# Performance work log

Measured on AMD Instinct MI355X. Metric: run time of the kernel, lower is better.

The kernel has to match this reference:

```python
import jax, jax.numpy as jnp
import numpy as np

INPUT_DIM = 362
HIDDEN = 256
STYLE_NUM = 60
OUTFIT_NUM = 49710
BATCH = 16384


def setup_inputs() -> dict:
    key = jax.random.key(0)
    ks = jax.random.split(key, 12)
    f32 = jnp.float32
    return {
        "i_feature": jax.random.normal(ks[0], (BATCH, INPUT_DIM), f32),
        "j_feature": jax.random.normal(ks[1], (BATCH, INPUT_DIM), f32),
        "k_feature": jax.random.normal(ks[2], (BATCH, INPUT_DIM), f32),
        # top_emb / bottom_emb Linear params (stored transposed: x @ W + b)
        "W_top": jax.random.normal(ks[3], (INPUT_DIM, HIDDEN), f32) * 0.05,
        "b_top": jnp.zeros((HIDDEN,), f32),
        "W_bot": jax.random.normal(ks[4], (INPUT_DIM, HIDDEN), f32) * 0.05,
        "b_bot": jnp.zeros((HIDDEN,), f32),
        # NMF factors (forward relu_'s them in place; we relu on use)
        "P_nmf": jax.random.normal(ks[5], (2 * INPUT_DIM, STYLE_NUM), f32),
        "N_nmf": jax.random.normal(ks[6], (2 * INPUT_DIM, STYLE_NUM), f32),
        "H1_nmf": jax.random.normal(ks[7], (STYLE_NUM, OUTFIT_NUM), f32),
        "H2_nmf": jax.random.normal(ks[8], (STYLE_NUM, OUTFIT_NUM), f32),
        "matirx_pos": jax.random.uniform(ks[9], (2 * INPUT_DIM, OUTFIT_NUM), f32),
        "matirx_neg": jax.random.uniform(ks[10], (2 * INPUT_DIM, OUTFIT_NUM), f32),
    }


def _emb(x, W, b):
    # nn.Sequential(Linear, Sigmoid)
    return jax.nn.sigmoid(x @ W + b)


def _style_score(i_f, j_f, styles, W_top, b_top, W_bot, b_bot):
    # Vectorized version of the per-sample loop:
    # squared-distance argmin codebook lookup + gather + rowwise dot.
    outfit = jnp.concatenate([i_f, j_f], axis=1)  # [B, 2D]
    # mean over feature dim of (x - s)^2; constant 1/(2D) scale does not change argmin
    d2 = (jnp.sum(outfit * outfit, axis=1, keepdims=True)
          - 2.0 * (outfit @ styles)
          + jnp.sum(styles * styles, axis=0, keepdims=True))  # [B, S]
    idx = jnp.argmin(d2, axis=1)                               # [B]
    sel = styles.T[idx]                                        # [B, 2D] gather
    top, bot = sel[:, :INPUT_DIM], sel[:, INPUT_DIM:]
    # diag(matmul) == rowwise dot
    return jnp.sum(_emb(top, W_top, b_top) * _emb(bot, W_bot, b_bot), axis=1)  # [B]


def reference(i_feature, j_feature, k_feature, W_top, b_top, W_bot, b_bot,
              P_nmf, N_nmf, H1_nmf, H2_nmf, matirx_pos, matirx_neg):
    Ti = _emb(i_feature, W_top, b_top)   # [B, H]
    Bj = _emb(j_feature, W_bot, b_bot)   # [B, H]
    Bk = _emb(k_feature, W_bot, b_bot)   # [B, H]
    # torch.diag(matmul(Ti, Bj.T)) == rowwise dot (avoids [B,B] intermediate)
    ij_score = jnp.sum(Ti * Bj, axis=1)  # [B]
    ik_score = jnp.sum(Ti * Bk, axis=1)  # [B]

    # forward does relu_ on .data before use
    P = jnp.maximum(P_nmf, 0.0)
    N = jnp.maximum(N_nmf, 0.0)
    H1 = jnp.maximum(H1_nmf, 0.0)
    H2 = jnp.maximum(H2_nmf, 0.0)

    style_ij = _style_score(i_feature, j_feature, P, W_top, b_top, W_bot, b_bot)
    style_ik = _style_score(i_feature, k_feature, N, W_top, b_top, W_bot, b_bot)

    # -mean(log(sigmoid(d))) computed stably
    loss1 = -jnp.mean(jax.nn.log_sigmoid(ij_score - ik_score))
    loss2 = -jnp.mean(jax.nn.log_sigmoid(style_ij - style_ik))
    loss3 = jnp.mean(jnp.square(matirx_pos - P @ H1)
                     + jnp.square(matirx_neg - N @ H2))
    loss = loss1 + loss2 + 0.1 * loss3

    ij_ik = jnp.stack([ij_score, ik_score], axis=1)  # [B, 2]
    auc = jnp.mean((jnp.argmax(ij_ik, axis=1) == 0).astype(jnp.float32))
    return (loss, loss1, loss2, loss3, auc)
```

## Files before the change

kernel.cpp:

```cpp
#include <hip/hip_runtime.h>
#include <math.h>

#define BATCH 16384
#define IND   362
#define KP    384
#define HID   256
#define STY   60
#define NOUT  49710
#define OUTP  49792
#define D2    724
#define D2P   768
#define NSTRIP 777
#define L3_BLOCKS (2 * NSTRIP)

#define NB_SS   120
#define NB_CH   390
#define NB_CW   768
#define NB_CPN  384
#define NB_CF   9216
#define NB_PREP (NB_SS + NB_CH + NB_CW + NB_CPN + NB_CF)

#define NB_EMB  512
#define NB_SA   512
#define NB_MAIN (L3_BLOCKS + NB_EMB + NB_SA)

typedef __bf16 bf16x8 __attribute__((ext_vector_type(8)));
typedef float  floatx4 __attribute__((ext_vector_type(4)));
typedef float  floatx2 __attribute__((ext_vector_type(2)));

__device__ inline floatx4 mfma16(bf16x8 a, bf16x8 b, floatx4 c) {
  return __builtin_amdgcn_mfma_f32_16x16x32_bf16(a, b, c, 0, 0, 0);
}

__device__ inline unsigned short f32_to_bf16(float x) {
  unsigned int u = __float_as_uint(x);
  unsigned int r = (u + 0x7FFFu + ((u >> 16) & 1u)) >> 16;
  return (unsigned short)r;
}

__device__ inline float sigm_fast(float x) { return 1.0f / (1.0f + __expf(-x)); }
__device__ inline float softplusf(float z) { return fmaxf(z, 0.0f) + log1pf(expf(-fabsf(z))); }

__global__ __launch_bounds__(256) void k_prep(
    const float* __restrict__ fi, const float* __restrict__ fj, const float* __restrict__ fk,
    const float* __restrict__ Wt, const float* __restrict__ btop,
    const float* __restrict__ Wb, const float* __restrict__ bbot,
    const float* __restrict__ Pn, const float* __restrict__ Nn,
    const float* __restrict__ H1, const float* __restrict__ H2,
    unsigned short* __restrict__ fbf, unsigned short* __restrict__ wbfT,
    unsigned short* __restrict__ pnbf, unsigned short* __restrict__ pnbfT,
    unsigned short* __restrict__ hbfT,
    float* __restrict__ ss, float* __restrict__ cn) {
  __shared__ float sel[D2];
  __shared__ float shr[4];
  int b = blockIdx.x;
  int t = threadIdx.x;

  if (b < NB_SS) {
    int s  = b % STY;
    int mt = b / STY;
    const float* M = mt ? Nn : Pn;
    float cnp = 0.0f;
    for (int d = t; d < D2; d += 256) {
      float v = fmaxf(M[(size_t)d * STY + s], 0.0f);
      sel[d] = v;
      cnp += v * v;
    }
    __syncthreads();
    float at = btop[t], ab = bbot[t];
    for (int d = 0; d < IND; d++) at = fmaf(sel[d],       Wt[(size_t)d * HID + t], at);
    for (int d = 0; d < IND; d++) ab = fmaf(sel[IND + d], Wb[(size_t)d * HID + t], ab);
    float prod = (1.0f / (1.0f + expf(-at))) * (1.0f / (1.0f + expf(-ab)));
    for (int off = 32; off > 0; off >>= 1) prod += __shfl_xor(prod, off);
    if ((t & 63) == 0) shr[t >> 6] = prod;
    __syncthreads();
    if (t == 0) ss[mt * 64 + s] = shr[0] + shr[1] + shr[2] + shr[3];
    __syncthreads();
    for (int off = 32; off > 0; off >>= 1) cnp += __shfl_xor(cnp, off);
    if ((t & 63) == 0) shr[t >> 6] = cnp;
    __syncthreads();
    if (t == 0) cn[mt * 64 + s] = shr[0] + shr[1] + shr[2] + shr[3];
    return;
  }
  b -= NB_SS;

  if (b < NB_CH) {
    int o = (b % 195) * 256 + t;
    int m = b / 195;
    if (o >= OUTP) return;
    const float* H = m ? H2 : H1;
    unsigned short* dst = hbfT + ((size_t)m * OUTP + o) * 64;
    bool ov = (o < NOUT);
    #pragma unroll
    for (int g = 0; g < 8; g++) {
      unsigned int wv[4];
      #pragma unroll
      for (int e = 0; e < 4; e++) {
        int kk = g * 8 + e * 2;
        float lo = (ov && kk < STY)     ? fmaxf(H[(size_t)kk * NOUT + o], 0.0f) : 0.0f;
        float hi = (ov && kk + 1 < STY) ? fmaxf(H[(size_t)(kk + 1) * NOUT + o], 0.0f) : 0.0f;
        wv[e] = (unsigned)f32_to_bf16(lo) | ((unsigned)f32_to_bf16(hi) << 16);
      }
      uint4 v; v.x = wv[0]; v.y = wv[1]; v.z = wv[2]; v.w = wv[3];
      *(uint4*)(dst + g * 8) = v;
    }
    return;
  }
  b -= NB_CH;

  if (b < NB_CW) {
    int idx = b * 256 + t;
    int k = idx % KP;
    int rem = idx / KP;
    int h = rem % HID;
    int mm = rem / HID;
    const float* W = mm ? Wb : Wt;
    wbfT[idx] = f32_to_bf16(k < IND ? W[(size_t)k * HID + h] : 0.0f);
    return;
  }
  b -= NB_CW;

  if (b < NB_CPN) {
    int u = b * 256 + t;
    int s = u & 63;
    int v = u >> 6;
    int m = (v >= D2P) ? 1 : 0;
    int d = v - m * D2P;
    const float* M = m ? Nn : Pn;
    float x = (d < D2 && s < STY) ? fmaxf(M[(size_t)d * STY + s], 0.0f) : 0.0f;
    unsigned short bb = f32_to_bf16(x);
    pnbf[((size_t)m * D2P + d) * 64 + s] = bb;
    int k = (d < IND) ? d : (d < D2 ? d + 22 : (d < 746 ? d - IND : d));
    pnbfT[((size_t)m * 64 + s) * D2P + k] = bb;
    return;
  }
  b -= NB_CPN;

  {
    long u = (long)b * 256 + t;
    int g = (int)(u % 48);
    long rf = u / 48;
    int row = (int)(rf % BATCH);
    int f = (int)(rf / BATCH);
    const float* src = (f == 0) ? fi : (f == 1 ? fj : fk);
    int d0 = g * 8;
    const float* sp = src + (size_t)row * IND + d0;
    unsigned int wv[4];
    #pragma unroll
    for (int e = 0; e < 4; e++) {
      int dd = d0 + 2 * e;
      float lo = (dd < IND)     ? sp[2 * e]     : 0.0f;
      float hi = (dd + 1 < IND) ? sp[2 * e + 1] : 0.0f;
      wv[e] = (unsigned)f32_to_bf16(lo) | ((unsigned)f32_to_bf16(hi) << 16);
    }
    uint4 v; v.x = wv[0]; v.y = wv[1]; v.z = wv[2]; v.w = wv[3];
    *(uint4*)(fbf + ((size_t)f * BATCH + row) * KP + d0) = v;
  }
}

__global__ __launch_bounds__(256) void k_main(
    const unsigned short* __restrict__ fbf, const unsigned short* __restrict__ wbfT,
    const unsigned short* __restrict__ pnbf, const unsigned short* __restrict__ pnbfT,
    const unsigned short* __restrict__ hbfT,
    const float* __restrict__ btop, const float* __restrict__ bbot,
    const float* __restrict__ cn, const float* __restrict__ ss,
    const float* __restrict__ mp, const float* __restrict__ mn,
    float* __restrict__ sIJ, float* __restrict__ sIK,
    float* __restrict__ stIJ, float* __restrict__ stIK,
    float* __restrict__ partial) {
  __shared__ float shp[4];
  int w = threadIdx.x >> 6, lane = threadIdx.x & 63;
  int m = lane & 15, q = lane >> 4;
  int b = blockIdx.x;

  if (b < L3_BLOCKS) {
    int strip = b % NSTRIP;
    int mat   = b / NSTRIP;
    int o0 = strip * 64;
    const float* M = mat ? mn : mp;
    const unsigned short* Hb = hbfT + (size_t)mat * OUTP * 64;
    const unsigned short* Pb = pnbf + (size_t)mat * D2P * 64;

    bf16x8 a[4][2];
    #pragma unroll
    for (int t = 0; t < 4; t++)
      #pragma unroll
      for (int kc = 0; kc < 2; kc++)
        a[t][kc] = *(const bf16x8*)(Hb + (size_t)(o0 + t * 16 + m) * 64 + kc * 32 + q * 8);

    bool full = (o0 + 64 <= NOUT);
    float local = 0.0f;
    floatx2 pcur[8], pnxt[8];
    #pragma unroll
    for (int i = 0; i < 8; i++) { pcur[i] = (floatx2){0.f, 0.f}; pnxt[i] = (floatx2){0.f, 0.f}; }

    auto LOAD = [&](int dt, floatx2* dst) {
      int d = dt * 16 + m;
      if (d < D2) {
        const float* Mrow = M + (size_t)d * NOUT + o0;
        if (full) {
          #pragma unroll
          for (int t = 0; t < 4; t++) {
            int ob = t * 16 + q * 4;
            dst[2 * t]     = *(const floatx2*)(Mrow + ob);
            dst[2 * t + 1] = *(const floatx2*)(Mrow + ob + 2);
          }
        } else {
          #pragma unroll
          for (int t = 0; t < 4; t++) {
            int ob = t * 16 + q * 4;
            floatx2 v0 = {0.f, 0.f}, v1 = {0.f, 0.f};
            if (o0 + ob     < NOUT) v0[0] = Mrow[ob];
            if (o0 + ob + 1 < NOUT) v0[1] = Mrow[ob + 1];
            if (o0 + ob + 2 < NOUT) v1[0] = Mrow[ob + 2];
            if (o0 + ob + 3 < NOUT) v1[1] = Mrow[ob + 3];
            dst[2 * t] = v0; dst[2 * t + 1] = v1;
          }
        }
      }
    };

    LOAD(w, pcur);
    for (int dt = w; dt < 46; dt += 4) {
      if (dt + 4 < 46) LOAD(dt + 4, pnxt);
      int d0 = dt * 16;
      const unsigned short* bp = Pb + (size_t)(d0 + m) * 64 + q * 8;
      bf16x8 b0 = *(const bf16x8*)(bp);
      bf16x8 b1 = *(const bf16x8*)(bp + 32);
      floatx4 acc[4];
      #pragma unroll
      for (int t = 0; t < 4; t++) {
        acc[t] = (floatx4){0.f, 0.f, 0.f, 0.f};
        acc[t] = mfma16(a[t][0], b0, acc[t]);
        acc[t] = mfma16(a[t][1], b1, acc[t]);
      }
      if (d0 + m < D2) {
        #pragma unroll
        for (int t = 0; t < 4; t++) {
          float e0 = pcur[2 * t][0]     - acc[t][0];
          float e1 = pcur[2 * t][1]     - acc[t][1];
          float e2 = pcur[2 * t + 1][0] - acc[t][2];
          float e3 = pcur[2 * t + 1][1] - acc[t][3];
          local += e0 * e0 + e1 * e1 + e2 * e2 + e3 * e3;
        }
      }
      #pragma unroll
      for (int i = 0; i < 8; i++) pcur[i] = pnxt[i];
    }
    for (int off = 32; off > 0; off >>= 1) local += __shfl_xor(local, off);
    if (lane == 0) shp[w] = local;
    __syncthreads();
    if (threadIdx.x == 0) partial[b] = shp[0] + shp[1] + shp[2] + shp[3];
    return;
  }
  b -= L3_BLOCKS;

  if (b < NB_EMB) {
    int r0 = (b & 255) * 64 + w * 16;
    int hb = (b >> 8) * 128;
    const unsigned short* fi = fbf + (size_t)(r0 + m) * KP + q * 8;
    const unsigned short* fj = fi + (size_t)BATCH * KP;
    const unsigned short* fk = fj + (size_t)BATCH * KP;
    floatx4 accI[8], accJ[8], accK[8];
    #pragma unroll
    for (int nt = 0; nt < 8; nt++) {
      accI[nt] = (floatx4){0.f, 0.f, 0.f, 0.f};
      accJ[nt] = (floatx4){0.f, 0.f, 0.f, 0.f};
      accK[nt] = (floatx4){0.f, 0.f, 0.f, 0.f};
    }
    for (int kc = 0; kc < 12; kc++) {
      bf16x8 ai = *(const bf16x8*)(fi + kc * 32);
      bf16x8 aj = *(const bf16x8*)(fj + kc * 32);
      bf16x8 ak = *(const bf16x8*)(fk + kc * 32);
      #pragma unroll
      for (int nt = 0; nt < 8; nt++) {
        int n = hb + nt * 16 + m;
        const unsigned short* wp = wbfT + (size_t)n * KP + kc * 32 + q * 8;
        bf16x8 bt8 = *(const bf16x8*)(wp);
        bf16x8 bb8 = *(const bf16x8*)(wp + (size_t)HID * KP);
        accI[nt] = mfma16(ai, bt8, accI[nt]);
        accJ[nt] = mfma16(aj, bb8, accJ[nt]);
        accK[nt] = mfma16(ak, bb8, accK[nt]);
      }
    }
    float sij[4] = {0.f, 0.f, 0.f, 0.f}, sik[4] = {0.f, 0.f, 0.f, 0.f};
    #pragma unroll
    for (int nt = 0; nt < 8; nt++) {
      int n = hb + nt * 16 + m;
      float vbt = btop[n], vbb = bbot[n];
      #pragma unroll
      for (int reg = 0; reg < 4; reg++) {
        float ti = sigm_fast(accI[nt][reg] + vbt);
        float tj = sigm_fast(accJ[nt][reg] + vbb);
        float tk = sigm_fast(accK[nt][reg] + vbb);
        sij[reg] += ti * tj;
        sik[reg] += ti * tk;
      }
    }
    #pragma unroll
    for (int reg = 0; reg < 4; reg++) {
      for (int off = 1; off < 16; off <<= 1) {
        sij[reg] += __shfl_xor(sij[reg], off);
        sik[reg] += __shfl_xor(sik[reg], off);
      }
    }
    if (m == 0) {
      #pragma unroll
      for (int reg = 0; reg < 4; reg++) {
        int row = r0 + q * 4 + reg;
        atomicAdd(&sIJ[row], sij[reg]);
        atomicAdd(&sIK[row], sik[reg]);
      }
    }
    return;
  }
  b -= NB_EMB;

  {
    int mat = w & 1;
    int r0 = b * 32 + (w >> 1) * 16;
    const unsigned short* fA = fbf + (size_t)(r0 + m) * KP + q * 8;
    const unsigned short* fB = fA + (size_t)(1 + mat) * BATCH * KP;
    const unsigned short* Bp = pnbfT + (size_t)mat * 64 * D2P + q * 8;
    floatx4 acc[4];
    #pragma unroll
    for (int nt = 0; nt < 4; nt++) acc[nt] = (floatx4){0.f, 0.f, 0.f, 0.f};
    for (int kc = 0; kc < 24; kc++) {
      bf16x8 a = (kc < 12) ? *(const bf16x8*)(fA + kc * 32)
                           : *(const bf16x8*)(fB + (kc - 12) * 32);
      #pragma unroll
      for (int nt = 0; nt < 4; nt++) {
        bf16x8 bb = *(const bf16x8*)(Bp + (size_t)(nt * 16 + m) * D2P + kc * 32);
        acc[nt] = mfma16(a, bb, acc[nt]);
      }
    }
    const float* cnm = cn + mat * 64;
    float bv[4]; int bi[4];
    #pragma unroll
    for (int reg = 0; reg < 4; reg++) { bv[reg] = __builtin_inff(); bi[reg] = 1 << 30; }
    #pragma unroll
    for (int nt = 0; nt < 4; nt++) {
      int s = nt * 16 + m;
      float c = cnm[s & 63];
      #pragma unroll
      for (int reg = 0; reg < 4; reg++) {
        float d2 = (s < STY) ? (c - 2.0f * acc[nt][reg]) : __builtin_inff();
        if (d2 < bv[reg] || (d2 == bv[reg] && s < bi[reg])) { bv[reg] = d2; bi[reg] = s; }
      }
    }
    for (int off = 1; off < 16; off <<= 1) {
      #pragma unroll
      for (int reg = 0; reg < 4; reg++) {
        float ov = __shfl_xor(bv[reg], off);
        int   oi = __shfl_xor(bi[reg], off);
        if (ov < bv[reg] || (ov == bv[reg] && oi < bi[reg])) { bv[reg] = ov; bi[reg] = oi; }
      }
    }
    if (m == 0) {
      float* dst = mat ? stIK : stIJ;
      const float* ssm = ss + mat * 64;
      #pragma unroll
      for (int reg = 0; reg < 4; reg++) dst[r0 + q * 4 + reg] = ssm[bi[reg]];
    }
  }
}

__global__ __launch_bounds__(256) void k_final(
    const float* __restrict__ sIJ, const float* __restrict__ sIK,
    const float* __restrict__ stIJ, const float* __restrict__ stIK,
    const float* __restrict__ l3partial, float* __restrict__ out) {
  int t = threadIdx.x;
  float l1 = 0.f, l2 = 0.f, ac = 0.f;
  for (int r = t; r < BATCH; r += 256) {
    float dij = sIJ[r] - sIK[r];
    l1 += softplusf(-dij);
    if (dij >= 0.0f) ac += 1.0f;
    float dst = stIJ[r] - stIK[r];
    l2 += softplusf(-dst);
  }
  double l3 = 0.0;
  for (int p = t; p < L3_BLOCKS; p += 256) l3 += (double)l3partial[p];
  __shared__ float sh1[4], sh2[4], sh3[4];
  __shared__ double sh4[4];
  for (int off = 32; off > 0; off >>= 1) {
    l1 += __shfl_xor(l1, off);
    l2 += __shfl_xor(l2, off);
    ac += __shfl_xor(ac, off);
    l3 += __shfl_xor(l3, off);
  }
  if ((t & 63) == 0) { sh1[t >> 6] = l1; sh2[t >> 6] = l2; sh3[t >> 6] = ac; sh4[t >> 6] = l3; }
  __syncthreads();
  if (t == 0) {
    double L1 = 0, L2 = 0, AC = 0, L3 = 0;
    for (int i = 0; i < 4; i++) { L1 += sh1[i]; L2 += sh2[i]; AC += sh3[i]; L3 += sh4[i]; }
    L1 /= BATCH; L2 /= BATCH; AC /= BATCH;
    L3 /= ((double)D2 * (double)NOUT);
    out[0] = (float)(L1 + L2 + 0.1 * L3);
    out[1] = (float)L1;
    out[2] = (float)L2;
    out[3] = (float)L3;
    out[4] = (float)AC;
  }
}

extern "C" void kernel_launch(void* const* d_in, const int* in_sizes, int n_in,
                              void* d_out, int out_size, void* d_ws, size_t ws_size,
                              hipStream_t stream) {
  (void)in_sizes; (void)n_in; (void)out_size; (void)ws_size;
  const float* i_f  = (const float*)d_in[0];
  const float* j_f  = (const float*)d_in[1];
  const float* k_f  = (const float*)d_in[2];
  const float* W_t  = (const float*)d_in[3];
  const float* b_t  = (const float*)d_in[4];
  const float* W_b  = (const float*)d_in[5];
  const float* b_b  = (const float*)d_in[6];
  const float* P_n  = (const float*)d_in[7];
  const float* N_n  = (const float*)d_in[8];
  const float* H1   = (const float*)d_in[9];
  const float* H2   = (const float*)d_in[10];
  const float* Mp   = (const float*)d_in[11];
  const float* Mn   = (const float*)d_in[12];
  float* out = (float*)d_out;
  char* ws = (char*)d_ws;

  const size_t OFF_FBF   = 0;
  const size_t OFF_WBFT  = OFF_FBF  + (size_t)3 * BATCH * KP * 2;
  const size_t OFF_PNBF  = OFF_WBFT + (size_t)2 * HID * KP * 2;
  const size_t OFF_PNBFT = OFF_PNBF + (size_t)2 * D2P * 64 * 2;
  const size_t OFF_HBFT  = OFF_PNBFT+ (size_t)2 * 64 * D2P * 2;
  const size_t OFF_SIJ   = OFF_HBFT + (size_t)2 * OUTP * 64 * 2;
  const size_t OFF_SIK   = OFF_SIJ  + (size_t)BATCH * 4;
  const size_t OFF_STIJ  = OFF_SIK  + (size_t)BATCH * 4;
  const size_t OFF_STIK  = OFF_STIJ + (size_t)BATCH * 4;
  const size_t OFF_SS    = OFF_STIK + (size_t)BATCH * 4;
  const size_t OFF_CN    = OFF_SS   + 512;
  const size_t OFF_L3P   = OFF_CN   + 512;

  unsigned short* fbf   = (unsigned short*)(ws + OFF_FBF);
  unsigned short* wbfT  = (unsigned short*)(ws + OFF_WBFT);
  unsigned short* pnbf  = (unsigned short*)(ws + OFF_PNBF);
  unsigned short* pnbfT = (unsigned short*)(ws + OFF_PNBFT);
  unsigned short* hbfT  = (unsigned short*)(ws + OFF_HBFT);
  float*  sIJ  = (float*)(ws + OFF_SIJ);
  float*  sIK  = (float*)(ws + OFF_SIK);
  float*  stIJ = (float*)(ws + OFF_STIJ);
  float*  stIK = (float*)(ws + OFF_STIK);
  float*  ss   = (float*)(ws + OFF_SS);
  float*  cn   = (float*)(ws + OFF_CN);
  float*  l3p  = (float*)(ws + OFF_L3P);

  hipMemsetAsync(ws + OFF_SIJ, 0, (size_t)BATCH * 4 * 2, stream);

  k_prep<<<NB_PREP, 256, 0, stream>>>(i_f, j_f, k_f, W_t, b_t, W_b, b_b,
                                      P_n, N_n, H1, H2,
                                      fbf, wbfT, pnbf, pnbfT, hbfT, ss, cn);
  k_main<<<NB_MAIN, 256, 0, stream>>>(fbf, wbfT, pnbf, pnbfT, hbfT,
                                      b_t, b_b, cn, ss, Mp, Mn,
                                      sIJ, sIK, stIJ, stIK, l3p);
  k_final<<<1, 256, 0, stream>>>(sIJ, sIK, stIJ, stIK, l3p, out);
}
```

Before: 641.0 us.

## Expand NMF reconstruction loss algebraically via Gram matrices instead of forming P@H

The loss3 term is rewritten as sum(M^2) - 2*sum(P ⊙ (M·H^T)) + <P^T P, H H^T>. This avoids reconstructing P@H at every element. The main blocks now stream M once, computing M·H^T with MFMA over output chunks. Extra head blocks compute the 64x64 Gram matrices H·H^T and P^T·P, which are combined in the final kernel. H is also stored row-major in bf16, the embedding blocks are split to a smaller hidden tile, and occupancy hints are added. The risks are cancellation error from subtracting large terms and global atomics from the few long-running head blocks.

```diff
diff --git a/kernel.cpp b/kernel.cpp
--- a/kernel.cpp
+++ b/kernel.cpp
@@ -7,22 +7,27 @@
 #define HID   256
 #define STY   60
 #define NOUT  49710
-#define OUTP  49792
+#define OUTP  49920
 #define D2    724
 #define D2P   768
-#define NSTRIP 777
-#define L3_BLOCKS (2 * NSTRIP)
 
 #define NB_SS   120
-#define NB_CH   390
+#define NB_HR   3120
 #define NB_CW   768
 #define NB_CPN  384
 #define NB_CF   9216
-#define NB_PREP (NB_SS + NB_CH + NB_CW + NB_CPN + NB_CF)
-
-#define NB_EMB  512
+#define NB_PREP (NB_SS + NB_HR + NB_CW + NB_CPN + NB_CF)
+
+#define NB_HH   16
+#define NB_PPB  2
+#define NB_HEAD (NB_HH + NB_PPB)
+#define N_DT    46
+#define N_OC    24
+#define OCHUNK  2080
+#define NB_M    (2 * N_DT * N_OC)
+#define NB_EMB  1024
 #define NB_SA   512
-#define NB_MAIN (L3_BLOCKS + NB_EMB + NB_SA)
+#define NB_MAIN (NB_HEAD + NB_M + NB_EMB + NB_SA)
 
 typedef __bf16 bf16x8 __attribute__((ext_vector_type(8)));
 typedef float  floatx4 __attribute__((ext_vector_type(4)));
@@ -48,8 +53,7 @@
     const float* __restrict__ Pn, const float* __restrict__ Nn,
     const float* __restrict__ H1, const float* __restrict__ H2,
     unsigned short* __restrict__ fbf, unsigned short* __restrict__ wbfT,
-    unsigned short* __restrict__ pnbf, unsigned short* __restrict__ pnbfT,
-    unsigned short* __restrict__ hbfT,
+    unsigned short* __restrict__ pnbfT, unsigned short* __restrict__ hrows,
     float* __restrict__ ss, float* __restrict__ cn) {
   __shared__ float sel[D2];
   __shared__ float shr[4];
@@ -84,29 +88,36 @@
   }
   b -= NB_SS;
 
-  if (b < NB_CH) {
-    int o = (b % 195) * 256 + t;
-    int m = b / 195;
-    if (o >= OUTP) return;
-    const float* H = m ? H2 : H1;
-    unsigned short* dst = hbfT + ((size_t)m * OUTP + o) * 64;
-    bool ov = (o < NOUT);
-    #pragma unroll
-    for (int g = 0; g < 8; g++) {
-      unsigned int wv[4];
-      #pragma unroll
-      for (int e = 0; e < 4; e++) {
-        int kk = g * 8 + e * 2;
-        float lo = (ov && kk < STY)     ? fmaxf(H[(size_t)kk * NOUT + o], 0.0f) : 0.0f;
-        float hi = (ov && kk + 1 < STY) ? fmaxf(H[(size_t)(kk + 1) * NOUT + o], 0.0f) : 0.0f;
-        wv[e] = (unsigned)f32_to_bf16(lo) | ((unsigned)f32_to_bf16(hi) << 16);
-      }
-      uint4 v; v.x = wv[0]; v.y = wv[1]; v.z = wv[2]; v.w = wv[3];
-      *(uint4*)(dst + g * 8) = v;
-    }
-    return;
-  }
-  b -= NB_CH;
+  if (b < NB_HR) {
+    int e = (b * 256 + t) * 8;
+    int row = e / OUTP;
+    int o = e - row * OUTP;
+    int s = row & 63;
+    int mm = row >> 6;
+    const float* H = mm ? H2 : H1;
+    unsigned short* dst = hrows + (size_t)row * OUTP + o;
+    unsigned int wv[4];
+    if (s < STY && o + 8 <= NOUT) {
+      const float* src = H + (size_t)s * NOUT + o;
+      #pragma unroll
+      for (int ee = 0; ee < 4; ee++) {
+        floatx2 v = *(const floatx2*)(src + 2 * ee);
+        wv[ee] = (unsigned)f32_to_bf16(fmaxf(v[0], 0.0f)) |
+                 ((unsigned)f32_to_bf16(fmaxf(v[1], 0.0f)) << 16);
+      }
+    } else {
+      #pragma unroll
+      for (int ee = 0; ee < 4; ee++) {
+        float lo = (s < STY && o + 2 * ee     < NOUT) ? fmaxf(H[(size_t)s * NOUT + o + 2 * ee],     0.0f) : 0.0f;
+        float hi = (s < STY && o + 2 * ee + 1 < NOUT) ? fmaxf(H[(size_t)s * NOUT + o + 2 * ee + 1], 0.0f) : 0.0f;
+        wv[ee] = (unsigned)f32_to_bf16(lo) | ((unsigned)f32_to_bf16(hi) << 16);
+      }
+    }
+    uint4 v; v.x = wv[0]; v.y = wv[1]; v.z = wv[2]; v.w = wv[3];
+    *(uint4*)dst = v;
+    return;
+  }
+  b -= NB_HR;
 
   if (b < NB_CW) {
     int idx = b * 256 + t;
@@ -129,7 +140,6 @@
     const float* M = m ? Nn : Pn;
     float x = (d < D2 && s < STY) ? fmaxf(M[(size_t)d * STY + s], 0.0f) : 0.0f;
     unsigned short bb = f32_to_bf16(x);
-    pnbf[((size_t)m * D2P + d) * 64 + s] = bb;
     int k = (d < IND) ? d : (d < D2 ? d + 22 : (d < 746 ? d - IND : d));
     pnbfT[((size_t)m * 64 + s) * D2P + k] = bb;
     return;
@@ -158,112 +168,176 @@
   }
 }
 
-__global__ __launch_bounds__(256) void k_main(
+__global__ __launch_bounds__(256, 4) void k_main(
     const unsigned short* __restrict__ fbf, const unsigned short* __restrict__ wbfT,
-    const unsigned short* __restrict__ pnbf, const unsigned short* __restrict__ pnbfT,
-    const unsigned short* __restrict__ hbfT,
+    const unsigned short* __restrict__ pnbfT, const unsigned short* __restrict__ hrows,
     const float* __restrict__ btop, const float* __restrict__ bbot,
     const float* __restrict__ cn, const float* __restrict__ ss,
-    const float* __restrict__ mp, const float* __restrict__ mn,
+    const float* __restrict__ mp, const float* __restrict__ mneg,
+    const float* __restrict__ Pn, const float* __restrict__ Nn,
     float* __restrict__ sIJ, float* __restrict__ sIK,
     float* __restrict__ stIJ, float* __restrict__ stIK,
+    float* __restrict__ HHb, float* __restrict__ PPb,
     float* __restrict__ partial) {
   __shared__ float shp[4];
+  __shared__ float red[4096];
   int w = threadIdx.x >> 6, lane = threadIdx.x & 63;
   int m = lane & 15, q = lane >> 4;
   int b = blockIdx.x;
 
-  if (b < L3_BLOCKS) {
-    int strip = b % NSTRIP;
-    int mat   = b / NSTRIP;
-    int o0 = strip * 64;
-    const float* M = mat ? mn : mp;
-    const unsigned short* Hb = hbfT + (size_t)mat * OUTP * 64;
-    const unsigned short* Pb = pnbf + (size_t)mat * D2P * 64;
-
-    bf16x8 a[4][2];
-    #pragma unroll
-    for (int t = 0; t < 4; t++)
-      #pragma unroll
-      for (int kc = 0; kc < 2; kc++)
-        a[t][kc] = *(const bf16x8*)(Hb + (size_t)(o0 + t * 16 + m) * 64 + kc * 32 + q * 8);
-
-    bool full = (o0 + 64 <= NOUT);
-    float local = 0.0f;
-    floatx2 pcur[8], pnxt[8];
-    #pragma unroll
-    for (int i = 0; i < 8; i++) { pcur[i] = (floatx2){0.f, 0.f}; pnxt[i] = (floatx2){0.f, 0.f}; }
-
-    auto LOAD = [&](int dt, floatx2* dst) {
-      int d = dt * 16 + m;
-      if (d < D2) {
-        const float* Mrow = M + (size_t)d * NOUT + o0;
+  if (b < NB_HEAD) {
+    bool isPP = (b >= NB_HH);
+    int mat, chunk, nsteps, stride;
+    const unsigned short* Rb;
+    if (!isPP) { mat = b >> 3; chunk = b & 7; Rb = hrows + (size_t)mat * 64 * OUTP; stride = OUTP; nsteps = 195; }
+    else       { mat = b - NB_HH; chunk = 0; Rb = pnbfT + (size_t)mat * 64 * D2P;  stride = D2P;  nsteps = 24;  }
+    const unsigned short* Rm = Rb + (size_t)m * stride;
+
+    floatx4 acc[4][4];
+    #pragma unroll
+    for (int a2 = 0; a2 < 4; a2++)
+      #pragma unroll
+      for (int b2 = 0; b2 < 4; b2++) acc[a2][b2] = (floatx4){0.f, 0.f, 0.f, 0.f};
+
+    bf16x8 hc[4], hn[4];
+    auto LD = [&](int j, bf16x8* h) {
+      int k = (chunk * nsteps + j) * 32 + q * 8;
+      #pragma unroll
+      for (int st = 0; st < 4; st++)
+        h[st] = *(const bf16x8*)(Rm + (size_t)(st * 16) * stride + k);
+    };
+    int j = w;
+    LD(j, hc);
+    for (; j < nsteps; j += 4) {
+      if (j + 4 < nsteps) LD(j + 4, hn);
+      #pragma unroll
+      for (int a2 = 0; a2 < 4; a2++)
+        #pragma unroll
+        for (int b2 = 0; b2 < 4; b2++)
+          acc[a2][b2] = mfma16(hc[a2], hc[b2], acc[a2][b2]);
+      #pragma unroll
+      for (int st = 0; st < 4; st++) hc[st] = hn[st];
+    }
+    for (int idx = threadIdx.x; idx < 4096; idx += 256) red[idx] = 0.f;
+    __syncthreads();
+    #pragma unroll
+    for (int a2 = 0; a2 < 4; a2++)
+      #pragma unroll
+      for (int b2 = 0; b2 < 4; b2++)
+        #pragma unroll
+        for (int r = 0; r < 4; r++)
+          atomicAdd(&red[(a2 * 16 + q * 4 + r) * 64 + b2 * 16 + m], acc[a2][b2][r]);
+    __syncthreads();
+    float* dst = (isPP ? PPb : HHb) + (size_t)mat * 4096;
+    for (int idx = threadIdx.x; idx < 4096; idx += 256) atomicAdd(&dst[idx], red[idx]);
+    return;
+  }
+  b -= NB_HEAD;
+
+  if (b < NB_M) {
+    int dt  = b % N_DT;
+    int r   = b / N_DT;
+    int oc  = r % N_OC;
+    int mat = r / N_OC;
+    int d0 = dt * 16, o0 = oc * OCHUNK;
+    bool full = (o0 + OCHUNK <= NOUT);
+    int d = d0 + m;
+    bool rowok = (d < D2);
+    const float* Mrow = (mat ? mneg : mp) + (size_t)d * NOUT;
+    const unsigned short* Hbase = hrows + ((size_t)mat * 64 + m) * OUTP;
+
+    floatx4 acc[4];
+    #pragma unroll
+    for (int st = 0; st < 4; st++) acc[st] = (floatx4){0.f, 0.f, 0.f, 0.f};
+    float msq = 0.0f;
+
+    floatx2 mc[4], mnx[4];
+    bf16x8  hc[4], hn[4];
+
+    auto LOADM = [&](int j, floatx2* dst) {
+      int o = o0 + j * 32 + q * 8;
+      if (rowok) {
+        const float* Mr = Mrow + o;
         if (full) {
-          #pragma unroll
-          for (int t = 0; t < 4; t++) {
-            int ob = t * 16 + q * 4;
-            dst[2 * t]     = *(const floatx2*)(Mrow + ob);
-            dst[2 * t + 1] = *(const floatx2*)(Mrow + ob + 2);
-          }
+          dst[0] = *(const floatx2*)(Mr);
+          dst[1] = *(const floatx2*)(Mr + 2);
+          dst[2] = *(const floatx2*)(Mr + 4);
+          dst[3] = *(const floatx2*)(Mr + 6);
         } else {
           #pragma unroll
-          for (int t = 0; t < 4; t++) {
-            int ob = t * 16 + q * 4;
-            floatx2 v0 = {0.f, 0.f}, v1 = {0.f, 0.f};
-            if (o0 + ob     < NOUT) v0[0] = Mrow[ob];
-            if (o0 + ob + 1 < NOUT) v0[1] = Mrow[ob + 1];
-            if (o0 + ob + 2 < NOUT) v1[0] = Mrow[ob + 2];
-            if (o0 + ob + 3 < NOUT) v1[1] = Mrow[ob + 3];
-            dst[2 * t] = v0; dst[2 * t + 1] = v1;
+          for (int e = 0; e < 4; e++) {
+            floatx2 v = {0.f, 0.f};
+            if (o + 2 * e     < NOUT) v[0] = Mr[2 * e];
+            if (o + 2 * e + 1 < NOUT) v[1] = Mr[2 * e + 1];
+            dst[e] = v;
           }
         }
+      } else {
+        #pragma unroll
+        for (int e = 0; e < 4; e++) dst[e] = (floatx2){0.f, 0.f};
       }
     };
-
-    LOAD(w, pcur);
-    for (int dt = w; dt < 46; dt += 4) {
-      if (dt + 4 < 46) LOAD(dt + 4, pnxt);
-      int d0 = dt * 16;
-      const unsigned short* bp = Pb + (size_t)(d0 + m) * 64 + q * 8;
-      bf16x8 b0 = *(const bf16x8*)(bp);
-      bf16x8 b1 = *(const bf16x8*)(bp + 32);
-      floatx4 acc[4];
-      #pragma unroll
-      for (int t = 0; t < 4; t++) {
-        acc[t] = (floatx4){0.f, 0.f, 0.f, 0.f};
-        acc[t] = mfma16(a[t][0], b0, acc[t]);
-        acc[t] = mfma16(a[t][1], b1, acc[t]);
-      }
-      if (d0 + m < D2) {
+    auto LOADH = [&](int j, bf16x8* h) {
+      int o = o0 + j * 32 + q * 8;
+      #pragma unroll
+      for (int st = 0; st < 4; st++)
+        h[st] = *(const bf16x8*)(Hbase + (size_t)(st * 16) * OUTP + o);
+    };
+
+    LOADM(w, mc);
+    LOADH(w, hc);
+    for (int j = w; j < 65; j += 4) {
+      if (j + 4 < 65) { LOADM(j + 4, mnx); LOADH(j + 4, hn); }
+      union { unsigned int u32[4]; bf16x8 v; } cv;
+      #pragma unroll
+      for (int e = 0; e < 4; e++) {
+        msq = fmaf(mc[e][0], mc[e][0], msq);
+        msq = fmaf(mc[e][1], mc[e][1], msq);
+        cv.u32[e] = (unsigned)f32_to_bf16(mc[e][0]) | ((unsigned)f32_to_bf16(mc[e][1]) << 16);
+      }
+      bf16x8 af = cv.v;
+      #pragma unroll
+      for (int st = 0; st < 4; st++) acc[st] = mfma16(af, hc[st], acc[st]);
+      #pragma unroll
+      for (int e = 0; e < 4; e++) mc[e] = mnx[e];
+      #pragma unroll
+      for (int st = 0; st < 4; st++) hc[st] = hn[st];
+    }
+
+    const float* PM = mat ? Nn : Pn;
+    float t2 = 0.0f;
+    #pragma unroll
+    for (int st = 0; st < 4; st++) {
+      int s = st * 16 + m;
+      if (s < STY) {
         #pragma unroll
-        for (int t = 0; t < 4; t++) {
-          float e0 = pcur[2 * t][0]     - acc[t][0];
-          float e1 = pcur[2 * t][1]     - acc[t][1];
-          float e2 = pcur[2 * t + 1][0] - acc[t][2];
-          float e3 = pcur[2 * t + 1][1] - acc[t][3];
-          local += e0 * e0 + e1 * e1 + e2 * e2 + e3 * e3;
+        for (int rg = 0; rg < 4; rg++) {
+          int dd = d0 + q * 4 + rg;
+          if (dd < D2) {
+            float pv = fmaxf(PM[(size_t)dd * STY + s], 0.0f);
+            t2 = fmaf(pv, acc[st][rg], t2);
+          }
         }
       }
-      #pragma unroll
-      for (int i = 0; i < 8; i++) pcur[i] = pnxt[i];
-    }
+    }
+    float local = msq - 2.0f * t2;
     for (int off = 32; off > 0; off >>= 1) local += __shfl_xor(local, off);
     if (lane == 0) shp[w] = local;
     __syncthreads();
     if (threadIdx.x == 0) partial[b] = shp[0] + shp[1] + shp[2] + shp[3];
     return;
   }
-  b -= L3_BLOCKS;
+  b -= NB_M;
 
   if (b < NB_EMB) {
     int r0 = (b & 255) * 64 + w * 16;
-    int hb = (b >> 8) * 128;
+    int hb = (b >> 8) * 64;
     const unsigned short* fi = fbf + (size_t)(r0 + m) * KP + q * 8;
     const unsigned short* fj = fi + (size_t)BATCH * KP;
     const unsigned short* fk = fj + (size_t)BATCH * KP;
-    floatx4 accI[8], accJ[8], accK[8];
-    #pragma unroll
-    for (int nt = 0; nt < 8; nt++) {
+    floatx4 accI[4], accJ[4], accK[4];
+    #pragma unroll
+    for (int nt = 0; nt < 4; nt++) {
       accI[nt] = (floatx4){0.f, 0.f, 0.f, 0.f};
       accJ[nt] = (floatx4){0.f, 0.f, 0.f, 0.f};
       accK[nt] = (floatx4){0.f, 0.f, 0.f, 0.f};
@@ -273,7 +347,7 @@
       bf16x8 aj = *(const bf16x8*)(fj + kc * 32);
       bf16x8 ak = *(const bf16x8*)(fk + kc * 32);
       #pragma unroll
-      for (int nt = 0; nt < 8; nt++) {
+      for (int nt = 0; nt < 4; nt++) {
         int n = hb + nt * 16 + m;
         const unsigned short* wp = wbfT + (size_t)n * KP + kc * 32 + q * 8;
         bf16x8 bt8 = *(const bf16x8*)(wp);
@@ -285,7 +359,7 @@
     }
     float sij[4] = {0.f, 0.f, 0.f, 0.f}, sik[4] = {0.f, 0.f, 0.f, 0.f};
     #pragma unroll
-    for (int nt = 0; nt < 8; nt++) {
+    for (int nt = 0; nt < 4; nt++) {
       int n = hb + nt * 16 + m;
       float vbt = btop[n], vbb = bbot[n];
       #pragma unroll
@@ -368,7 +442,9 @@
 __global__ __launch_bounds__(256) void k_final(
     const float* __restrict__ sIJ, const float* __restrict__ sIK,
     const float* __restrict__ stIJ, const float* __restrict__ stIK,
-    const float* __restrict__ l3partial, float* __restrict__ out) {
+    const float* __restrict__ l3partial,
+    const float* __restrict__ HHb, const float* __restrict__ PPb,
+    float* __restrict__ out) {
   int t = threadIdx.x;
   float l1 = 0.f, l2 = 0.f, ac = 0.f;
   for (int r = t; r < BATCH; r += 256) {
@@ -379,7 +455,8 @@
     l2 += softplusf(-dst);
   }
   double l3 = 0.0;
-  for (int p = t; p < L3_BLOCKS; p += 256) l3 += (double)l3partial[p];
+  for (int p = t; p < NB_M; p += 256) l3 += (double)l3partial[p];
+  for (int idx = t; idx < 8192; idx += 256) l3 += (double)HHb[idx] * (double)PPb[idx];
   __shared__ float sh1[4], sh2[4], sh3[4];
   __shared__ double sh4[4];
   for (int off = 32; off > 0; off >>= 1) {
@@ -424,38 +501,40 @@
   char* ws = (char*)d_ws;
 
   const size_t OFF_FBF   = 0;
-  const size_t OFF_WBFT  = OFF_FBF  + (size_t)3 * BATCH * KP * 2;
-  const size_t OFF_PNBF  = OFF_WBFT + (size_t)2 * HID * KP * 2;
-  const size_t OFF_PNBFT = OFF_PNBF + (size_t)2 * D2P * 64 * 2;
-  const size_t OFF_HBFT  = OFF_PNBFT+ (size_t)2 * 64 * D2P * 2;
-  const size_t OFF_SIJ   = OFF_HBFT + (size_t)2 * OUTP * 64 * 2;
-  const size_t OFF_SIK   = OFF_SIJ  + (size_t)BATCH * 4;
-  const size_t OFF_STIJ  = OFF_SIK  + (size_t)BATCH * 4;
-  const size_t OFF_STIK  = OFF_STIJ + (size_t)BATCH * 4;
-  const size_t OFF_SS    = OFF_STIK + (size_t)BATCH * 4;
-  const size_t OFF_CN    = OFF_SS   + 512;
-  const size_t OFF_L3P   = OFF_CN   + 512;
+  const size_t OFF_WBFT  = OFF_FBF   + (size_t)3 * BATCH * KP * 2;
+  const size_t OFF_PNBFT = OFF_WBFT  + (size_t)2 * HID * KP * 2;
+  const size_t OFF_HROWS = OFF_PNBFT + (size_t)2 * 64 * D2P * 2;
+  const size_t OFF_SIJ   = OFF_HROWS + (size_t)2 * 64 * OUTP * 2;
+  const size_t OFF_SIK   = OFF_SIJ   + (size_t)BATCH * 4;
+  const size_t OFF_HH    = OFF_SIK   + (size_t)BATCH * 4;
+  const size_t OFF_PP    = OFF_HH    + (size_t)2 * 4096 * 4;
+  const size_t OFF_STIJ  = OFF_PP    + (size_t)2 * 4096 * 4;
+  const size_t OFF_STIK  = OFF_STIJ  + (size_t)BATCH * 4;
+  const size_t OFF_SS    = OFF_STIK  + (size_t)BATCH * 4;
+  const size_t OFF_CN    = OFF_SS    + 512;
+  const size_t OFF_L3P   = OFF_CN    + 512;
 
   unsigned short* fbf   = (unsigned short*)(ws + OFF_FBF);
   unsigned short* wbfT  = (unsigned short*)(ws + OFF_WBFT);
-  unsigned short* pnbf  = (unsigned short*)(ws + OFF_PNBF);
   unsigned short* pnbfT = (unsigned short*)(ws + OFF_PNBFT);
-  unsigned short* hbfT  = (unsigned short*)(ws + OFF_HBFT);
+  unsigned short* hrows = (unsigned short*)(ws + OFF_HROWS);
   float*  sIJ  = (float*)(ws + OFF_SIJ);
   float*  sIK  = (float*)(ws + OFF_SIK);
+  float*  HHb  = (float*)(ws + OFF_HH);
+  float*  PPb  = (float*)(ws + OFF_PP);
   float*  stIJ = (float*)(ws + OFF_STIJ);
   float*  stIK = (float*)(ws + OFF_STIK);
   float*  ss   = (float*)(ws + OFF_SS);
   float*  cn   = (float*)(ws + OFF_CN);
   float*  l3p  = (float*)(ws + OFF_L3P);
 
-  hipMemsetAsync(ws + OFF_SIJ, 0, (size_t)BATCH * 4 * 2, stream);
+  hipMemsetAsync(ws + OFF_SIJ, 0, (size_t)BATCH * 4 * 2 + (size_t)4 * 4096 * 4, stream);
 
   k_prep<<<NB_PREP, 256, 0, stream>>>(i_f, j_f, k_f, W_t, b_t, W_b, b_b,
                                       P_n, N_n, H1, H2,
-                                      fbf, wbfT, pnbf, pnbfT, hbfT, ss, cn);
-  k_main<<<NB_MAIN, 256, 0, stream>>>(fbf, wbfT, pnbf, pnbfT, hbfT,
-                                      b_t, b_b, cn, ss, Mp, Mn,
-                                      sIJ, sIK, stIJ, stIK, l3p);
-  k_final<<<1, 256, 0, stream>>>(sIJ, sIK, stIJ, stIK, l3p, out);
+                                      fbf, wbfT, pnbfT, hrows, ss, cn);
+  k_main<<<NB_MAIN, 256, 0, stream>>>(fbf, wbfT, pnbfT, hrows,
+                                      b_t, b_b, cn, ss, Mp, Mn, P_n, N_n,
+                                      sIJ, sIK, stIJ, stIK, HHb, PPb, l3p);
+  k_final<<<1, 256, 0, stream>>>(sIJ, sIK, stIJ, stIK, l3p, HHb, PPb, out);
 }
```

Result: slower. 662.8 us (+3.4%).
